# Performance work log

Hardware: AMD Instinct MI355X
Metric: run time of the kernel (lower is better)

The kernel has to match this reference:

```python
import jax, jax.numpy as jnp
import numpy as np

# Config (from ModelConfig in source; num_layers reduced to 4 for the reference)
B, T, D = 4, 8192, 1024
P = 512            # num_patches
S = 4              # patch_stride (OverlapAddDecoder upsample factor)
L = 4              # num transformer layers
NH, NKV, HD = 16, 4, 64
FF = 4096          # ffn_multiplier * D
KC = 256           # MoD capacity = 0.5 * P
V = 257            # vocab_size


def rmsnorm(x, w, eps=1e-6):
    return x * jax.lax.rsqrt(jnp.mean(x * x, -1, keepdims=True) + eps) * w


def rope_cache(n, d):
    theta = 1.0 / (10000.0 ** (jnp.arange(0, d, 2, dtype=jnp.float32) / d))
    fr = jnp.arange(n, dtype=jnp.float32)[:, None] * theta[None, :]
    e = jnp.concatenate([fr, fr], -1)
    return jnp.cos(e), jnp.sin(e)  # (n, d) each


def rot_half(x):
    h = x.shape[-1] // 2
    return jnp.concatenate([-x[..., h:], x[..., :h]], -1)


def setup_inputs() -> dict:
    key = jax.random.key(0)
    ks = iter(jax.random.split(key, 40))
    n = lambda s: jax.random.normal(next(ks), s, dtype=jnp.float32) * 0.02
    return {
        'tokens': jax.random.randint(next(ks), (B, T), 0, V),
        'emb': n((V, D)),
        'bp_w1': n((D // 2, D, 3)), 'bp_b1': jnp.zeros((D // 2,), jnp.float32),
        'bp_w2': n((1, D // 2, 3)), 'bp_b2': jnp.zeros((1,), jnp.float32),
        'enc_norm_w': jnp.ones((D,), jnp.float32),
        'router_w': n((L, D)),
        'ln1_w': jnp.ones((L, D), jnp.float32), 'ln2_w': jnp.ones((L, D), jnp.float32),
        'q_w': n((L, D, D)), 'k_w': n((L, D, NKV * HD)), 'v_w': n((L, D, NKV * HD)), 'o_w': n((L, D, D)),
        'gate_w': n((L, D, FF)), 'up_w': n((L, D, FF)), 'down_w': n((L, FF, D)),
        'dec_proj_w': n((D, S * D)), 'dec_proj_b': jnp.zeros((S * D,), jnp.float32),
        'dec_mlp_w1': n((D, D // 4)), 'dec_mlp_b1': jnp.zeros((D // 4,), jnp.float32),
        'dec_mlp_w2': n((D // 4, S)), 'dec_mlp_b2': jnp.zeros((S,), jnp.float32),
        'dec_norm_w': jnp.ones((D,), jnp.float32),
        'head_w': n((D, V)),
    }


def reference(tokens, emb, bp_w1, bp_b1, bp_w2, bp_b2, enc_norm_w, router_w,
              ln1_w, ln2_w, q_w, k_w, v_w, o_w, gate_w, up_w, down_w,
              dec_proj_w, dec_proj_b, dec_mlp_w1, dec_mlp_b1, dec_mlp_w2, dec_mlp_b2,
              dec_norm_w, head_w):
    x = emb[tokens]  # (B, T, D) byte embeddings

    # --- LearnedBoundaryPredictor: 2-layer 1D CNN -> per-segment soft boundaries ---
    dn = ('NCH', 'OIH', 'NCH')
    xT = x.transpose(0, 2, 1)  # (B, D, T)
    h1 = jax.lax.conv_general_dilated(xT, bp_w1, (1,), ((1, 1),), dimension_numbers=dn) + bp_b1[None, :, None]
    h1 = jax.nn.gelu(h1)
    lg = jax.lax.conv_general_dilated(h1, bp_w2, (1,), ((1, 1),), dimension_numbers=dn) + bp_b2[None, :, None]
    lg = lg[:, 0, :]  # (B, T)

    seg = T // P  # uniform segments (T divisible by P so all segments equal)
    lgw = jax.nn.softmax(lg.reshape(B, P, seg), -1)
    pos = jnp.arange(T, dtype=jnp.float32).reshape(P, seg)
    bp = jnp.sum(lgw * pos[None], -1)                                   # (B, P) soft boundary positions
    ent = -jnp.sum(lgw * jnp.log(jnp.clip(lgw, 1e-8)), -1) / np.log(seg)  # (B, P) entropy signal

    # --- gather patch embeddings at boundary positions, RMSNorm ---
    idx = jnp.clip(bp.astype(jnp.int32), 0, T - 1)
    patches = jnp.take_along_axis(x, idx[..., None], 1)  # (B, P, D)
    xp = rmsnorm(patches, enc_norm_w)

    cos, sin = rope_cache(P, HD)
    b_idx = jnp.arange(B)[:, None]
    causal = jnp.tril(jnp.ones((KC, KC), bool))
    G = NH // NKV

    # --- MoD-routed transformer stack: top-k tokens go through the layer ---
    for l in range(L):
        rl = jnp.einsum('bpd,d->bp', xp, router_w[l]) + ent  # router logits (entropy-boosted)
        _, sel = jax.lax.top_k(rl, KC)
        sel = jnp.sort(sel, -1)  # ascending positions -> causal order preserved
        xs = xp[b_idx, sel]      # (B, KC, D) selected tokens
        g = jax.nn.sigmoid(rl[b_idx, sel])[..., None]  # router gate
        cs = cos[sel][:, None]   # (B, 1, KC, HD)
        sn = sin[sel][:, None]

        # GQA with RoPE, causal
        h = rmsnorm(xs, ln1_w[l])
        q = (h @ q_w[l]).reshape(B, KC, NH, HD).transpose(0, 2, 1, 3)
        k = (h @ k_w[l]).reshape(B, KC, NKV, HD).transpose(0, 2, 1, 3)
        v = (h @ v_w[l]).reshape(B, KC, NKV, HD).transpose(0, 2, 1, 3)
        q = q * cs + rot_half(q) * sn
        k = k * cs + rot_half(k) * sn
        k = jnp.repeat(k, G, axis=1)
        v = jnp.repeat(v, G, axis=1)
        sc = jnp.einsum('bhqd,bhkd->bhqk', q, k) / np.sqrt(HD)
        sc = jnp.where(causal, sc, -1e30)
        a = jax.nn.softmax(sc, -1)
        ao = (jnp.einsum('bhqk,bhkd->bhqd', a, v).transpose(0, 2, 1, 3).reshape(B, KC, D)) @ o_w[l]

        x2 = xs + ao
        h2 = rmsnorm(x2, ln2_w[l])
        ff = (jax.nn.silu(h2 @ gate_w[l]) * (h2 @ up_w[l])) @ down_w[l]
        delta = ao + ff  # layer(x_sel) - x_sel
        xp = xp.at[b_idx, sel].add(g * delta)  # scatter back; unselected pass through

    # --- OverlapAddDecoder ---
    proj = (xp @ dec_proj_w + dec_proj_b).reshape(B, P, S, D)
    win = jax.nn.sigmoid(jax.nn.gelu(xp @ dec_mlp_w1 + dec_mlp_b1) @ dec_mlp_w2 + dec_mlp_b2)  # (B, P, S)
    out = rmsnorm((proj * win[..., None]).reshape(B, P * S, D), dec_norm_w)
    return out @ head_w  # (B, P*S, V) byte logits
```

## Files before the change

kernel.cpp:

```cpp
#include <hip/hip_runtime.h>
#include <hip/hip_bf16.h>
#include <math.h>

constexpr int Bn  = 4;
constexpr int Tn  = 8192;
constexpr int Dn  = 1024;
constexpr int Pn  = 512;
constexpr int SEGn= 16;
constexpr int Sn  = 4;
constexpr int Ln  = 4;
constexpr int NHn = 16;
constexpr int NKVn= 4;
constexpr int HDn = 64;
constexpr int FFn = 4096;
constexpr int KCn = 256;
constexpr int Vn  = 257;
constexpr int DHn = 512;

constexpr long OFF_EW  = 0;
constexpr long OFF_CA  = 394752;
constexpr long OFF_CB  = 427520;
constexpr long OFF_CC  = 460288;
constexpr long OFF_ENT = 493056;
constexpr long OFF_IDX = 495104;
constexpr long OFF_XP  = 497152;
constexpr long OFF_RL  = 2594304;
constexpr long OFF_SEL = 2596352;
constexpr long OFF_G   = 2597376;
constexpr long SCR     = 2598400;
constexpr long SC_XS   = 0;
constexpr long SC_H    = 1048576;
constexpr long SC_QKV  = 2097152;
constexpr long SC_AOUT = 3670016;
constexpr long SC_AO   = 4718592;
constexpr long SC_H2   = 5767168;
constexpr long SC_GU   = 6815744;
constexpr long SC_PROJ = 0;
constexpr long SC_Y    = 8921088;
constexpr long SC_EA   = 0;
constexpr long SC_WB   = 524288;
constexpr long OFF_WT    = 19908096;
constexpr long OFF_PARTS = 24102400;
constexpr long OFF_GHL   = 28820992;

typedef __attribute__((ext_vector_type(8))) short short8;
typedef __attribute__((ext_vector_type(4))) float floatx4;

__device__ __forceinline__ float geluf(float x) {
    float u = 0.7978845608028654f * (x + 0.044715f * x * x * x);
    float e = __expf(2.f * u);
    float t = 1.f - 2.f / (e + 1.f);
    return 0.5f * x * (1.f + t);
}
__device__ __forceinline__ float sigmf(float x) { return 1.f / (1.f + expf(-x)); }

__device__ __forceinline__ void cvt_hilo(float x, unsigned short& h, unsigned short& l) {
    unsigned u = __float_as_uint(x);
    h = (unsigned short)(u >> 16);
    float r = x - __uint_as_float(u & 0xffff0000u);
    l = (unsigned short)(__float_as_uint(r) >> 16);
}

typedef const __attribute__((address_space(1))) unsigned int* gas_p;
typedef __attribute__((address_space(3))) unsigned int* las_p;
__device__ __forceinline__ void gload16(const unsigned short* g, unsigned short* l) {
    __builtin_amdgcn_global_load_lds((gas_p)g, (las_p)l, 16, 0, 0);
}

__device__ __forceinline__ float blk_sum256(float v, float* red) {
    for (int o = 32; o > 0; o >>= 1) v += __shfl_down(v, o);
    int lane = threadIdx.x & 63, w = threadIdx.x >> 6;
    if (lane == 0) red[w] = v;
    __syncthreads();
    float r = red[0] + red[1] + red[2] + red[3];
    __syncthreads();
    return r;
}

__global__ void k_emb_pad(const float* __restrict__ emb, unsigned short* __restrict__ EA) {
    int i = blockIdx.x * blockDim.x + threadIdx.x;
    if (i >= 384 * 1024) return;
    int r = i >> 10, d = i & 1023;
    float v = (r < Vn) ? emb[r * 1024 + d] : 0.f;
    unsigned short hh, ll;
    cvt_hilo(v, hh, ll);
    EA[(long)r * 2048 + d] = hh;
    EA[(long)r * 2048 + 1024 + d] = ll;
}

__global__ void k_wconv_w1(const float* __restrict__ w1, unsigned short* __restrict__ WB) {
    int i = blockIdx.x * blockDim.x + threadIdx.x;
    if (i >= 1536 * 1024) return;
    int n = i >> 10, k = i & 1023;
    float v = w1[(n / 3) * 3072 + k * 3 + (n % 3)];
    unsigned short hh, ll;
    cvt_hilo(v, hh, ll);
    WB[(long)n * 2048 + k] = hh;
    WB[(long)n * 2048 + 1024 + k] = ll;
}

__global__ void k_ewred(const float* __restrict__ parts, float* __restrict__ EW) {
    int i = blockIdx.x * blockDim.x + threadIdx.x;
    if (i >= 3 * Vn * DHn) return;
    int dk = i / (Vn * DHn);
    int rem = i - dk * (Vn * DHn);
    int v = rem >> 9, o = rem & 511;
    long src = (long)v * 1536 + o * 3 + dk;
    float s = 0.f;
    constexpr long MN = 384L * 1536;
    #pragma unroll
    for (int c = 0; c < 8; c++) s += parts[c * MN + src];
    EW[i] = s;
}

__global__ void k_conv1(const int* __restrict__ tok, const float* __restrict__ EW,
                        const float* __restrict__ b1, const float* __restrict__ w2,
                        float* __restrict__ cA, float* __restrict__ cB, float* __restrict__ cC) {
    int wave = threadIdx.x >> 6, lane = threadIdx.x & 63;
    int gidx = blockIdx.x * 4 + wave;
    int b = gidx / Tn, t = gidx - b * Tn;
    int tk  = tok[b * Tn + t];
    int tkm = (t > 0)      ? tok[b * Tn + t - 1] : -1;
    int tkp = (t < Tn - 1) ? tok[b * Tn + t + 1] : -1;
    const float* E0 = EW;
    const float* E1 = EW + (long)Vn * DHn;
    const float* E2 = EW + 2L * Vn * DHn;
    float a0 = 0.f, a1 = 0.f, a2 = 0.f;
    #pragma unroll
    for (int u = 0; u < DHn / 64; u++) {
        int o = lane + u * 64;
        float s = b1[o] + E1[tk * DHn + o];
        if (tkm >= 0) s += E0[tkm * DHn + o];
        if (tkp >= 0) s += E2[tkp * DHn + o];
        float hg = geluf(s);
        a0 += hg * w2[o * 3 + 0];
        a1 += hg * w2[o * 3 + 1];
        a2 += hg * w2[o * 3 + 2];
    }
    for (int o = 32; o > 0; o >>= 1) {
        a0 += __shfl_down(a0, o); a1 += __shfl_down(a1, o); a2 += __shfl_down(a2, o);
    }
    if (lane == 0) { cA[gidx] = a0; cB[gidx] = a1; cC[gidx] = a2; }
}

__global__ void k_patchstats(const float* __restrict__ cA, const float* __restrict__ cB,
                             const float* __restrict__ cC, const float* __restrict__ b2,
                             float* __restrict__ ent_out, int* __restrict__ idx_out) {
    int pid = blockIdx.x * blockDim.x + threadIdx.x;
    if (pid >= Bn * Pn) return;
    int b = pid / Pn, p = pid - b * Pn;
    float lgv[SEGn];
    float m = -3.4e38f;
    for (int s = 0; s < SEGn; s++) {
        int t = p * SEGn + s;
        float v = b2[0] + cB[b * Tn + t];
        if (t > 0)      v += cA[b * Tn + t - 1];
        if (t < Tn - 1) v += cC[b * Tn + t + 1];
        lgv[s] = v; m = fmaxf(m, v);
    }
    float Z = 0.f;
    for (int s = 0; s < SEGn; s++) { lgv[s] = expf(lgv[s] - m); Z += lgv[s]; }
    float inv = 1.f / Z;
    float bp = 0.f, en = 0.f;
    for (int s = 0; s < SEGn; s++) {
        float w = lgv[s] * inv;
        bp += w * (float)(p * SEGn + s);
        en -= w * logf(fmaxf(w, 1e-8f));
    }
    en *= (1.f / 2.772588722239781f);
    ent_out[pid] = en;
    int ix = (int)bp;
    ix = ix < 0 ? 0 : (ix > Tn - 1 ? Tn - 1 : ix);
    idx_out[pid] = ix;
}

__global__ void k_xp(const int* __restrict__ tok, const int* __restrict__ idx,
                     const float* __restrict__ emb, const float* __restrict__ nw,
                     float* __restrict__ xp) {
    int pid = blockIdx.x;
    int b = pid / Pn;
    int tk = tok[b * Tn + idx[pid]];
    const float* row = emb + (long)tk * Dn;
    __shared__ float red[4];
    float v[4]; float ss = 0.f;
    #pragma unroll
    for (int j = 0; j < 4; j++) { v[j] = row[threadIdx.x + j * 256]; ss += v[j] * v[j]; }
    ss = blk_sum256(ss, red);
    float sc = 1.f / sqrtf(ss * (1.f / Dn) + 1e-6f);
    #pragma unroll
    for (int j = 0; j < 4; j++) {
        int d = threadIdx.x + j * 256;
        xp[(long)pid * Dn + d] = v[j] * sc * nw[d];
    }
}

__global__ void k_router(const float* __restrict__ xp, const float* __restrict__ rw,
                         const float* __restrict__ ent, float* __restrict__ rl) {
    int pid = blockIdx.x;
    const float* xr = xp + (long)pid * Dn;
    __shared__ float red[4];
    float s = 0.f;
    #pragma unroll
    for (int j = 0; j < 4; j++) { int d = threadIdx.x + j * 256; s += xr[d] * rw[d]; }
    s = blk_sum256(s, red);
    if (threadIdx.x == 0) rl[pid] = s + ent[pid];
}

__global__ void k_topk(const float* __restrict__ rl, int* __restrict__ sel, float* __restrict__ g) {
    int b = blockIdx.x, p = threadIdx.x;
    __shared__ float vals[Pn];
    __shared__ int flag[Pn];
    float v = rl[b * Pn + p];
    vals[p] = v;
    __syncthreads();
    int rank = 0;
    for (int q = 0; q < Pn; q++) {
        float vq = vals[q];
        rank += (vq > v || (vq == v && q < p)) ? 1 : 0;
    }
    int selected = rank < KCn ? 1 : 0;
    flag[p] = selected;
    __syncthreads();
    if (selected) {
        int pos = 0;
        for (int q = 0; q < p; q++) pos += flag[q];
        sel[b * KCn + pos] = p;
        g[b * KCn + pos] = sigmf(v);
    }
}

__global__ void k_gather_ln1(const float* __restrict__ xp, const int* __restrict__ sel,
                             const float* __restrict__ w, float* __restrict__ xs,
                             unsigned short* __restrict__ hHL) {
    int r = blockIdx.x;
    int b = r / KCn;
    int p = sel[r];
    const float* src = xp + ((long)b * Pn + p) * Dn;
    __shared__ float red[4];
    float v[4]; float ss = 0.f;
    #pragma unroll
    for (int j = 0; j < 4; j++) { v[j] = src[threadIdx.x + j * 256]; ss += v[j] * v[j]; }
    ss = blk_sum256(ss, red);
    float sc = 1.f / sqrtf(ss * (1.f / Dn) + 1e-6f);
    #pragma unroll
    for (int j = 0; j < 4; j++) {
        int d = threadIdx.x + j * 256;
        xs[(long)r * Dn + d] = v[j];
        unsigned short hh, ll;
        cvt_hilo(v[j] * sc * w[d], hh, ll);
        hHL[(long)r * 2048 + d] = hh;
        hHL[(long)r * 2048 + 1024 + d] = ll;
    }
}

__device__ __forceinline__ void wconv_body(const float* __restrict__ Wm,
                                           unsigned short* __restrict__ Whl,
                                           int K, int N, int roff, int n0, int k0) {
    __shared__ float t[32][33];
    int tx = threadIdx.x & 31, ty = threadIdx.x >> 5;
    #pragma unroll
    for (int r = 0; r < 4; r++) {
        int k = k0 + ty + 8 * r, n = n0 + tx;
        t[ty + 8 * r][tx] = (n < N) ? Wm[(long)k * N + n] : 0.f;
    }
    __syncthreads();
    long K2 = 2L * K;
    #pragma unroll
    for (int r = 0; r < 4; r++) {
        int n = n0 + ty + 8 * r, k = k0 + tx;
        float v = t[tx][ty + 8 * r];
        unsigned short hh, ll;
        cvt_hilo(v, hh, ll);
        Whl[(long)(roff + n) * K2 + k] = hh;
        Whl[(long)(roff + n) * K2 + K + k] = ll;
    }
}

__global__ void k_wconv(const float* __restrict__ Wm, unsigned short* __restrict__ Whl,
                        int K, int N, int roff) {
    wconv_body(Wm, Whl, K, N, roff, blockIdx.x * 32, blockIdx.y * 32);
}

__global__ void k_wconv2(const float* __restrict__ Wa, const float* __restrict__ Wb,
                         unsigned short* __restrict__ Whl, int K, int Nh) {
    int nb = Nh >> 5;
    int bx = blockIdx.x;
    const float* src = (bx < nb) ? Wa : Wb;
    int xb = (bx < nb) ? bx : bx - nb;
    int roff = (bx < nb) ? 0 : Nh;
    wconv_body(src, Whl, K, Nh, roff, xb * 32, blockIdx.y * 32);
}

__global__ void k_wconv_qkv(const float* __restrict__ qw, const float* __restrict__ kw,
                            const float* __restrict__ vw, unsigned short* __restrict__ Whl) {
    int bx = blockIdx.x;
    const float* src; int xb, roff, Nsrc;
    if (bx < 32)      { src = qw; xb = bx;      roff = 0;    Nsrc = 1024; }
    else if (bx < 40) { src = kw; xb = bx - 32; roff = 1024; Nsrc = 256; }
    else              { src = vw; xb = bx - 40; roff = 1280; Nsrc = 256; }
    wconv_body(src, Whl, 1024, Nsrc, roff, xb * 32, blockIdx.y * 32);
}

__global__ void k_xcvt(const float* __restrict__ src, unsigned short* __restrict__ dhl, int n) {
    int i = blockIdx.x * blockDim.x + threadIdx.x;
    if (i >= n) return;
    int r = i >> 10, d = i & 1023;
    unsigned short hh, ll;
    cvt_hilo(src[i], hh, ll);
    dhl[(long)r * 2048 + d] = hh;
    dhl[(long)r * 2048 + 1024 + d] = ll;
}

__global__ __launch_bounds__(256, 2) void k_mfma3(
        const unsigned short* __restrict__ Ag, const unsigned short* __restrict__ Bg,
        float* __restrict__ Cmat, const float* __restrict__ bias,
        int M, int N, int K, int splitK, float* __restrict__ parts) {
    __shared__ alignas(16) unsigned short As[2][128 * 64], Bs[2][128 * 64];
    int tid = threadIdx.x;
    int m0 = blockIdx.y * 128, n0 = blockIdx.x * 128;
    int kc = blockIdx.z;
    int Kc = K / splitK, kbase = kc * Kc, KT = Kc >> 5;
    int lane = tid & 63, wid = tid >> 6;
    int wm = (wid & 1) * 64, wn = (wid >> 1) * 64;
    int quad = lane >> 4, l16 = lane & 15;

    int srow8 = lane >> 3;
    int spos  = lane & 7;
    int cch   = spos ^ srow8;
    long K2 = 2L * K;
    long coff = (cch < 4) ? (long)(cch * 8) : (long)K + (long)((cch - 4) * 8);
    const unsigned short* Aseg = Ag + (long)(m0 + srow8) * K2 + coff;
    const unsigned short* Bseg = Bg + (long)(n0 + srow8) * K2 + coff;

    floatx4 acc[4][4];
    #pragma unroll
    for (int i = 0; i < 4; i++)
        #pragma unroll
        for (int j = 0; j < 4; j++) acc[i][j] = (floatx4){0.f, 0.f, 0.f, 0.f};

    auto stagef = [&](unsigned short* Ad, unsigned short* Bd, long kb) {
        #pragma unroll
        for (int t = 0; t < 4; t++) {
            int sa = wid * 4 + t;
            gload16(Aseg + (long)sa * 8 * K2 + kb, Ad + sa * 512);
            gload16(Bseg + (long)sa * 8 * K2 + kb, Bd + sa * 512);
        }
    };

    int ph = quad ^ (l16 & 7);
    stagef(As[0], Bs[0], kbase);
    __syncthreads();
    int cur = 0;
    for (int ks = 0; ks < KT; ks++) {
        if (ks + 1 < KT)
            stagef(As[cur ^ 1], Bs[cur ^ 1], kbase + (long)(ks + 1) * 32);

        const unsigned short* Ac = As[cur];
        const unsigned short* Bc = Bs[cur];
        short8 ah[4], al2[4], bh[4], bl2[4];
        #pragma unroll
        for (int i = 0; i < 4; i++) {
            int r = wm + i * 16 + l16;
            ah[i]  = *(const short8*)&Ac[r * 64 + ph * 8];
            al2[i] = *(const short8*)&Ac[r * 64 + (ph ^ 4) * 8];
        }
        #pragma unroll
        for (int j = 0; j < 4; j++) {
            int c = wn + j * 16 + l16;
            bh[j]  = *(const short8*)&Bc[c * 64 + ph * 8];
            bl2[j] = *(const short8*)&Bc[c * 64 + (ph ^ 4) * 8];
        }
        #pragma unroll
        for (int i = 0; i < 4; i++)
            #pragma unroll
            for (int j = 0; j < 4; j++) {
                acc[i][j] = __builtin_amdgcn_mfma_f32_16x16x32_bf16(ah[i],  bh[j],  acc[i][j], 0, 0, 0);
                acc[i][j] = __builtin_amdgcn_mfma_f32_16x16x32_bf16(ah[i],  bl2[j], acc[i][j], 0, 0, 0);
                acc[i][j] = __builtin_amdgcn_mfma_f32_16x16x32_bf16(al2[i], bh[j],  acc[i][j], 0, 0, 0);
            }
        __syncthreads();
        cur ^= 1;
    }

    long MN = (long)M * N;
    #pragma unroll
    for (int j = 0; j < 4; j++) {
        int n = n0 + wn + j * 16 + l16;
        if (n >= N) continue;
        float bvx = bias ? bias[n] : 0.f;
        #pragma unroll
        for (int i = 0; i < 4; i++) {
            int mb = m0 + wm + i * 16 + quad * 4;
            #pragma unroll
            for (int r = 0; r < 4; r++) {
                if (splitK > 1) parts[kc * MN + (long)(mb + r) * N + n] = acc[i][j][r];
                else            Cmat[(long)(mb + r) * N + n] = acc[i][j][r] + bvx;
            }
        }
    }
}

__global__ void k_reduce(const float* __restrict__ parts, float* __restrict__ out,
                         const float* __restrict__ bias, long MN, int sk, int N) {
    long i = (long)blockIdx.x * blockDim.x + threadIdx.x;
    if (i >= MN) return;
    float s = 0.f;
    for (int c = 0; c < sk; c++) s += parts[c * MN + i];
    if (bias) s += bias[(int)(i % N)];
    out[i] = s;
}

__global__ void k_qkv_finish(const float* __restrict__ parts, const int* __restrict__ sel,
                             float* __restrict__ qkv) {
    int r = blockIdx.x;
    int pos = sel[r];
    constexpr long MN = 1024L * 1536;
    #pragma unroll
    for (int it = 0; it < 3; it++) {
        int pp = threadIdx.x + it * 256;
        int head = pp >> 5, d = pp & 31;
        long c1 = (long)r * 1536 + head * 64 + d;
        float s1 = 0.f, s2 = 0.f;
        #pragma unroll
        for (int c = 0; c < 4; c++) {
            s1 += parts[c * MN + c1];
            s2 += parts[c * MN + c1 + 32];
        }
        if (head < 20) {
            float theta = powf(10000.f, -(float)(2 * d) / 64.f);
            float ang = (float)pos * theta;
            float cc = cosf(ang), ssn = sinf(ang);
            qkv[c1]      = s1 * cc - s2 * ssn;
            qkv[c1 + 32] = s2 * cc + s1 * ssn;
        } else {
            qkv[c1] = s1; qkv[c1 + 32] = s2;
        }
    }
}

constexpr int APS = 72;
__global__ __launch_bounds__(256) void k_attn(const float* __restrict__ qkv,
                       unsigned short* __restrict__ aoHL) {
    int bx = blockIdx.x, h = blockIdx.y, b = blockIdx.z;
    int hk = h >> 2;
    int qb0 = bx * 64;
    int tid = threadIdx.x, lane = tid & 63, wid = tid >> 6;
    int quad = lane >> 4, l16 = lane & 15;
    __shared__ alignas(16) unsigned short LdsA[9216], LdsB[9216];
    unsigned short* Kh = LdsA;          unsigned short* Kl = LdsB;
    unsigned short* Ph = LdsA;          unsigned short* Pl = LdsB;
    unsigned short* Vth = LdsA + 4608;  unsigned short* Vtl = LdsB + 4608;

    int qrow = qb0 + wid * 16 + l16;
    short8 qh[2], ql[2];
    #pragma unroll
    for (int ks = 0; ks < 2; ks++) {
        const float* qp = qkv + ((long)(b * KCn + qrow)) * 1536 + h * HDn + ks * 32 + quad * 8;
        float tmp[8];
        *(float4*)tmp = *(const float4*)qp;
        *(float4*)(tmp + 4) = *(const float4*)(qp + 4);
        #pragma unroll
        for (int j = 0; j < 8; j++) {
            unsigned short hh, ll;
            cvt_hilo(tmp[j], hh, ll);
            qh[ks][j] = (short)hh; ql[ks][j] = (short)ll;
        }
    }

    floatx4 sacc[16];
    #pragma unroll
    for (int t = 0; t < 16; t++) sacc[t] = (floatx4){0.f, 0.f, 0.f, 0.f};

    int qmax = qb0 + 63;
    int nkc = qmax / 128 + 1;
    for (int kc = 0; kc < nkc; kc++) {
        __syncthreads();
        {
            int r = tid >> 1, dh = (tid & 1) * 32;
            const float* kp = qkv + ((long)(b * KCn + kc * 128 + r)) * 1536 + 1024 + hk * HDn + dh;
            #pragma unroll
            for (int f = 0; f < 8; f++) {
                float tmp[4];
                *(float4*)tmp = *(const float4*)(kp + f * 4);
                unsigned short h0, h1, h2, h3, l0, l1, l2, l3;
                cvt_hilo(tmp[0], h0, l0); cvt_hilo(tmp[1], h1, l1);
                cvt_hilo(tmp[2], h2, l2); cvt_hilo(tmp[3], h3, l3);
                *(ushort4*)&Kh[r * APS + dh + f * 4] = make_ushort4(h0, h1, h2, h3);
                *(ushort4*)&Kl[r * APS + dh + f * 4] = make_ushort4(l0, l1, l2, l3);
            }
        }
        __syncthreads();
        #pragma unroll
        for (int tj = 0; tj < 8; tj++) {
            int kr = tj * 16 + l16;
            int gt = kc * 8 + tj;
            #pragma unroll
            for (int ks = 0; ks < 2; ks++) {
                short8 bh0 = *(const short8*)&Kh[kr * APS + ks * 32 + quad * 8];
                short8 bl0 = *(const short8*)&Kl[kr * APS + ks * 32 + quad * 8];
                sacc[gt] = __builtin_amdgcn_mfma_f32_16x16x32_bf16(qh[ks], bh0, sacc[gt], 0, 0, 0);
                sacc[gt] = __builtin_amdgcn_mfma_f32_16x16x32_bf16(qh[ks], bl0, sacc[gt], 0, 0, 0);
                sacc[gt] = __builtin_amdgcn_mfma_f32_16x16x32_bf16(ql[ks], bh0, sacc[gt], 0, 0, 0);
            }
        }
    }

    float rowinv[4];
    #pragma unroll
    for (int r = 0; r < 4; r++) {
        int qg = qb0 + wid * 16 + quad * 4 + r;
        float mm = -3.4e38f;
        #pragma unroll
        for (int t = 0; t < 16; t++) {
            int key = t * 16 + l16;
            float s = (key <= qg) ? sacc[t][r] * 0.125f : -1e30f;
            sacc[t][r] = s;
            mm = fmaxf(mm, s);
        }
        #pragma unroll
        for (int o = 1; o < 16; o <<= 1) mm = fmaxf(mm, __shfl_xor(mm, o));
        float zz = 0.f;
        #pragma unroll
        for (int t = 0; t < 16; t++) {
            float e = expf(sacc[t][r] - mm);
            sacc[t][r] = e; zz += e;
        }
        #pragma unroll
        for (int o = 1; o < 16; o <<= 1) zz += __shfl_xor(zz, o);
        rowinv[r] = 1.f / zz;
    }

    floatx4 oacc[4];
    #pragma unroll
    for (int dt = 0; dt < 4; dt++) oacc[dt] = (floatx4){0.f, 0.f, 0.f, 0.f};
    int npv = qmax / 64 + 1;
    for (int c4 = 0; c4 < npv; c4++) {
        __syncthreads();
        {
            #pragma unroll
            for (int it = 0; it < 4; it++) {
                int task = tid + 256 * it;
                int kloc = task & 63, d4 = (task >> 6) * 4;
                float tmp[4];
                *(float4*)tmp = *(const float4*)(qkv + ((long)(b * KCn + c4 * 64 + kloc)) * 1536 + 1280 + hk * HDn + d4);
                #pragma unroll
                for (int i = 0; i < 4; i++) {
                    unsigned short hh, ll;
                    cvt_hilo(tmp[i], hh, ll);
                    Vth[(d4 + i) * APS + kloc] = hh;
                    Vtl[(d4 + i) * APS + kloc] = ll;
                }
            }
        }
        #pragma unroll
        for (int tt = 0; tt < 4; tt++) {
            int t = c4 * 4 + tt;
            #pragma unroll
            for (int r = 0; r < 4; r++) {
                int row = wid * 16 + quad * 4 + r;
                float pv2 = sacc[t][r] * rowinv[r];
                unsigned short hh, ll;
                cvt_hilo(pv2, hh, ll);
                Ph[row * APS + tt * 16 + l16] = hh;
                Pl[row * APS + tt * 16 + l16] = ll;
            }
        }
        __syncthreads();
        short8 pah[2], pal[2];
        #pragma unroll
        for (int ks = 0; ks < 2; ks++) {
            pah[ks] = *(const short8*)&Ph[(wid * 16 + l16) * APS + ks * 32 + quad * 8];
            pal[ks] = *(const short8*)&Pl[(wid * 16 + l16) * APS + ks * 32 + quad * 8];
        }
        #pragma unroll
        for (int dt = 0; dt < 4; dt++) {
            #pragma unroll
            for (int ks = 0; ks < 2; ks++) {
                short8 vbh = *(const short8*)&Vth[(dt * 16 + l16) * APS + ks * 32 + quad * 8];
                short8 vbl = *(const short8*)&Vtl[(dt * 16 + l16) * APS + ks * 32 + quad * 8];
                oacc[dt] = __builtin_amdgcn_mfma_f32_16x16x32_bf16(pah[ks], vbh, oacc[dt], 0, 0, 0);
                oacc[dt] = __builtin_amdgcn_mfma_f32_16x16x32_bf16(pah[ks], vbl, oacc[dt], 0, 0, 0);
                oacc[dt] = __builtin_amdgcn_mfma_f32_16x16x32_bf16(pal[ks], vbh, oacc[dt], 0, 0, 0);
            }
        }
    }

    #pragma unroll
    for (int dt = 0; dt < 4; dt++) {
        #pragma unroll
        for (int r = 0; r < 4; r++) {
            int row = qb0 + wid * 16 + quad * 4 + r;
            long base = ((long)(b * KCn + row)) * 2048 + h * HDn + dt * 16 + l16;
            unsigned short hh, ll;
            cvt_hilo(oacc[dt][r], hh, ll);
            aoHL[base] = hh; aoHL[base + 1024] = ll;
        }
    }
}

__global__ void k_add_ln2_red(const float* __restrict__ parts, const float* __restrict__ xs,
                              const float* __restrict__ w, float* __restrict__ ao,
                              unsigned short* __restrict__ h2HL) {
    int r = blockIdx.x;
    constexpr long MN = 1024L * 1024;
    __shared__ float red[4];
    float v[4]; float ss = 0.f;
    #pragma unroll
    for (int j = 0; j < 4; j++) {
        int d = threadIdx.x + j * 256;
        long i = (long)r * Dn + d;
        float a = 0.f;
        #pragma unroll
        for (int c = 0; c < 8; c++) a += parts[c * MN + i];
        ao[i] = a;
        float x = xs[i] + a;
        v[j] = x; ss += x * x;
    }
    ss = blk_sum256(ss, red);
    float sc = 1.f / sqrtf(ss * (1.f / Dn) + 1e-6f);
    #pragma unroll
    for (int j = 0; j < 4; j++) {
        int d = threadIdx.x + j * 256;
        unsigned short hh, ll;
        cvt_hilo(v[j] * sc * w[d], hh, ll);
        h2HL[(long)r * 2048 + d] = hh;
        h2HL[(long)r * 2048 + 1024 + d] = ll;
    }
}

__global__ void k_silu_mul(const float* __restrict__ C, unsigned short* __restrict__ ghl, int n) {
    int i = blockIdx.x * blockDim.x + threadIdx.x;
    if (i < n) {
        int r = i >> 12, c = i & 4095;
        float x = C[(long)r * 8192 + c];
        float u = C[(long)r * 8192 + 4096 + c];
        unsigned short hh, ll;
        cvt_hilo(x * sigmf(x) * u, hh, ll);
        ghl[(long)r * 8192 + c] = hh;
        ghl[(long)r * 8192 + 4096 + c] = ll;
    }
}

__global__ void k_scatter_red(float* __restrict__ xp, const float* __restrict__ ao,
                              const float* __restrict__ parts, const float* __restrict__ g,
                              const int* __restrict__ sel) {
    int r = blockIdx.x;
    int b = r / KCn;
    int p = sel[r];
    float gg = g[r];
    constexpr long MN = 1024L * 1024;
    float* dst = xp + ((long)b * Pn + p) * Dn;
    #pragma unroll
    for (int j = 0; j < 4; j++) {
        int d = threadIdx.x + j * 256;
        long i = (long)r * Dn + d;
        float f = 0.f;
        #pragma unroll
        for (int c = 0; c < 4; c++) f += parts[c * MN + i];
        dst[d] += gg * (ao[i] + f);
    }
}

__global__ void k_dec_norm_win(const float* __restrict__ projC, const float* __restrict__ mparts,
                               const float* __restrict__ b1, const float* __restrict__ w2,
                               const float* __restrict__ b2, const float* __restrict__ w,
                               unsigned short* __restrict__ yHL) {
    int r = blockIdx.x;
    int bp = r >> 2, s = r & 3;
    constexpr long MN = 2048L * 256;
    __shared__ float red[4];
    long hi = (long)bp * 256 + threadIdx.x;
    float hv = b1[threadIdx.x];
    #pragma unroll
    for (int c = 0; c < 4; c++) hv += mparts[c * MN + hi];
    float acc = geluf(hv) * w2[threadIdx.x * 4 + s];
    acc = blk_sum256(acc, red);
    float wv = sigmf(acc + b2[s]);
    const float* pr = projC + (long)bp * 4096 + s * 1024;
    float v[4]; float ss = 0.f;
    #pragma unroll
    for (int j = 0; j < 4; j++) {
        int d = threadIdx.x + j * 256;
        float x = pr[d] * wv;
        v[j] = x; ss += x * x;
    }
    ss = blk_sum256(ss, red);
    float sc = 1.f / sqrtf(ss * (1.f / Dn) + 1e-6f);
    #pragma unroll
    for (int j = 0; j < 4; j++) {
        int d = threadIdx.x + j * 256;
        unsigned short hh, ll;
        cvt_hilo(v[j] * sc * w[d], hh, ll);
        yHL[(long)r * 2048 + d] = hh;
        yHL[(long)r * 2048 + 1024 + d] = ll;
    }
}

extern "C" void kernel_launch(void* const* d_in, const int* in_sizes, int n_in,
                              void* d_out, int out_size, void* d_ws, size_t ws_size,
                              hipStream_t stream) {
    const int*   tokens     = (const int*)  d_in[0];
    const float* emb        = (const float*)d_in[1];
    const float* bp_w1      = (const float*)d_in[2];
    const float* bp_b1      = (const float*)d_in[3];
    const float* bp_w2      = (const float*)d_in[4];
    const float* bp_b2      = (const float*)d_in[5];
    const float* enc_norm_w = (const float*)d_in[6];
    const float* router_w   = (const float*)d_in[7];
    const float* ln1_w      = (const float*)d_in[8];
    const float* ln2_w      = (const float*)d_in[9];
    const float* q_w        = (const float*)d_in[10];
    const float* k_w        = (const float*)d_in[11];
    const float* v_w        = (const float*)d_in[12];
    const float* o_w        = (const float*)d_in[13];
    const float* gate_w     = (const float*)d_in[14];
    const float* up_w       = (const float*)d_in[15];
    const float* down_w     = (const float*)d_in[16];
    const float* dec_proj_w = (const float*)d_in[17];
    const float* dec_proj_b = (const float*)d_in[18];
    const float* dec_mlp_w1 = (const float*)d_in[19];
    const float* dec_mlp_b1 = (const float*)d_in[20];
    const float* dec_mlp_w2 = (const float*)d_in[21];
    const float* dec_mlp_b2 = (const float*)d_in[22];
    const float* dec_norm_w = (const float*)d_in[23];
    const float* head_w     = (const float*)d_in[24];
    float* out = (float*)d_out;

    float* W = (float*)d_ws;
    float* EW   = W + OFF_EW;
    float* cA   = W + OFF_CA;
    float* cB   = W + OFF_CB;
    float* cC   = W + OFF_CC;
    float* ent  = W + OFF_ENT;
    int*   idxb = (int*)(W + OFF_IDX);
    float* xp   = W + OFF_XP;
    float* rl   = W + OFF_RL;
    int*   sel  = (int*)(W + OFF_SEL);
    float* g    = W + OFF_G;
    float* scr  = W + SCR;
    float* xs   = scr + SC_XS;
    unsigned short* hHL   = (unsigned short*)(scr + SC_H);
    float* qkv  = scr + SC_QKV;
    unsigned short* aoutHL = (unsigned short*)(scr + SC_AOUT);
    float* ao   = scr + SC_AO;
    unsigned short* h2HL  = (unsigned short*)(scr + SC_H2);
    float* gupC = scr + SC_GU;
    float* projC= scr + SC_PROJ;
    unsigned short* yHL   = (unsigned short*)(scr + SC_Y);
    unsigned short* EA    = (unsigned short*)(scr + SC_EA);
    unsigned short* WB    = (unsigned short*)(scr + SC_WB);
    unsigned short* WHL   = (unsigned short*)(W + OFF_WT);
    float* parts = W + OFF_PARTS;
    unsigned short* ghHL  = (unsigned short*)(W + OFF_GHL);
    unsigned short* xpHL  = (unsigned short*)(W + OFF_GHL);

    k_emb_pad<<<1536, 256, 0, stream>>>(emb, EA);
    k_wconv_w1<<<6144, 256, 0, stream>>>(bp_w1, WB);
    k_mfma3<<<dim3(12, 3, 8), 256, 0, stream>>>(EA, WB, nullptr, nullptr, 384, 1536, 1024, 8, parts);
    k_ewred<<<1542, 256, 0, stream>>>(parts, EW);
    k_conv1<<<Bn * Tn / 4, 256, 0, stream>>>(tokens, EW, bp_b1, bp_w2, cA, cB, cC);
    k_patchstats<<<(Bn * Pn + 255) / 256, 256, 0, stream>>>(cA, cB, cC, bp_b2, ent, idxb);
    k_xp<<<Bn * Pn, 256, 0, stream>>>(tokens, idxb, emb, enc_norm_w, xp);

    for (int l = 0; l < Ln; l++) {
        k_router<<<Bn * Pn, 256, 0, stream>>>(xp, router_w + (long)l * Dn, ent, rl);
        k_topk<<<Bn, Pn, 0, stream>>>(rl, sel, g);
        k_gather_ln1<<<Bn * KCn, 256, 0, stream>>>(xp, sel, ln1_w + (long)l * Dn, xs, hHL);

        k_wconv_qkv<<<dim3(48, 32), 256, 0, stream>>>(q_w + (long)l * Dn * Dn,
                                                      k_w + (long)l * Dn * 256,
                                                      v_w + (long)l * Dn * 256, WHL);
        k_mfma3<<<dim3(12, 8, 4), 256, 0, stream>>>(hHL, WHL, nullptr, nullptr, 1024, 1536, 1024, 4, parts);
        k_qkv_finish<<<Bn * KCn, 256, 0, stream>>>(parts, sel, qkv);

        k_attn<<<dim3(4, NHn, Bn), 256, 0, stream>>>(qkv, aoutHL);

        k_wconv<<<dim3(32, 32), 256, 0, stream>>>(o_w + (long)l * Dn * Dn, WHL, 1024, 1024, 0);
        k_mfma3<<<dim3(8, 8, 8), 256, 0, stream>>>(aoutHL, WHL, nullptr, nullptr, 1024, 1024, 1024, 8, parts);
        k_add_ln2_red<<<Bn * KCn, 256, 0, stream>>>(parts, xs, ln2_w + (long)l * Dn, ao, h2HL);

        k_wconv2<<<dim3(256, 32), 256, 0, stream>>>(gate_w + (long)l * Dn * FFn,
                                                    up_w + (long)l * Dn * FFn, WHL, 1024, 4096);
        k_mfma3<<<dim3(64, 8, 1), 256, 0, stream>>>(h2HL, WHL, gupC, nullptr, 1024, 8192, 1024, 1, parts);

        k_silu_mul<<<(Bn * KCn * FFn + 255) / 256, 256, 0, stream>>>(gupC, ghHL, Bn * KCn * FFn);

        k_wconv<<<dim3(32, 128), 256, 0, stream>>>(down_w + (long)l * FFn * Dn, WHL, 4096, 1024, 0);
        k_mfma3<<<dim3(8, 8, 4), 256, 0, stream>>>(ghHL, WHL, nullptr, nullptr, 1024, 1024, 4096, 4, parts);
        k_scatter_red<<<Bn * KCn, 256, 0, stream>>>(xp, ao, parts, g, sel);
    }

    k_xcvt<<<8192, 256, 0, stream>>>(xp, xpHL, 2097152);
    k_wconv<<<dim3(128, 32), 256, 0, stream>>>(dec_proj_w, WHL, 1024, 4096, 0);
    k_mfma3<<<dim3(32, 16, 1), 256, 0, stream>>>(xpHL, WHL, projC, dec_proj_b, 2048, 4096, 1024, 1, parts);
    k_wconv<<<dim3(8, 32), 256, 0, stream>>>(dec_mlp_w1, WHL, 1024, 256, 0);
    k_mfma3<<<dim3(2, 16, 4), 256, 0, stream>>>(xpHL, WHL, nullptr, nullptr, 2048, 256, 1024, 4, parts);
    k_dec_norm_win<<<Bn * Pn * Sn, 256, 0, stream>>>(projC, parts, dec_mlp_b1, dec_mlp_w2, dec_mlp_b2, dec_norm_w, yHL);
    k_wconv<<<dim3(9, 32), 256, 0, stream>>>(head_w, WHL, 1024, 257, 0);
    k_mfma3<<<dim3(3, 64, 2), 256, 0, stream>>>(yHL, WHL, nullptr, nullptr, 8192, 257, 1024, 2, parts);
    k_reduce<<<8224, 256, 0, stream>>>(parts, out, nullptr, 2105344, 2, 257);
}
```

Baseline: 1.437 ms.

## Store QKV pre-split as bf16 hi/lo, vectorize SiLU, raise down-proj split-K

k_qkv_finish now writes Q, K and V directly as bf16 hi/lo pairs in a split layout, so the attention kernel loads them with short8 copies instead of converting fp32 per element. The SiLU-mul kernel is vectorized to process four elements per thread. The down-projection GEMM goes from split-K 4 to 8, writing its partials into the gupC buffer, and the scatter reduction is updated to sum 8 partials. This trades extra partial-sum traffic for more parallelism in the down-projection, and relies on gupC being free to reuse at that point.

```diff
diff --git a/kernel.cpp b/kernel.cpp
--- a/kernel.cpp
+++ b/kernel.cpp
@@ -411,7 +411,7 @@
 }
 
 __global__ void k_qkv_finish(const float* __restrict__ parts, const int* __restrict__ sel,
-                             float* __restrict__ qkv) {
+                             unsigned short* __restrict__ qkvHL) {
     int r = blockIdx.x;
     int pos = sel[r];
     constexpr long MN = 1024L * 1536;
@@ -426,20 +426,33 @@
             s1 += parts[c * MN + c1];
             s2 += parts[c * MN + c1 + 32];
         }
+        float o1, o2;
         if (head < 20) {
             float theta = powf(10000.f, -(float)(2 * d) / 64.f);
             float ang = (float)pos * theta;
             float cc = cosf(ang), ssn = sinf(ang);
-            qkv[c1]      = s1 * cc - s2 * ssn;
-            qkv[c1 + 32] = s2 * cc + s1 * ssn;
+            o1 = s1 * cc - s2 * ssn;
+            o2 = s2 * cc + s1 * ssn;
         } else {
-            qkv[c1] = s1; qkv[c1 + 32] = s2;
-        }
+            o1 = s1; o2 = s2;
+        }
+        long hb, lb; int dloc;
+        if (head < 16)      { hb = 0;    lb = 1024; dloc = head * 64 + d; }
+        else if (head < 20) { hb = 2048; lb = 2304; dloc = (head - 16) * 64 + d; }
+        else                { hb = 2560; lb = 2816; dloc = (head - 20) * 64 + d; }
+        long base = (long)r * 3072;
+        unsigned short h1, l1, h2, l2;
+        cvt_hilo(o1, h1, l1);
+        cvt_hilo(o2, h2, l2);
+        qkvHL[base + hb + dloc]      = h1;
+        qkvHL[base + lb + dloc]      = l1;
+        qkvHL[base + hb + dloc + 32] = h2;
+        qkvHL[base + lb + dloc + 32] = l2;
     }
 }
 
 constexpr int APS = 72;
-__global__ __launch_bounds__(256) void k_attn(const float* __restrict__ qkv,
+__global__ __launch_bounds__(256) void k_attn(const unsigned short* __restrict__ qkvHL,
                        unsigned short* __restrict__ aoHL) {
     int bx = blockIdx.x, h = blockIdx.y, b = blockIdx.z;
     int hk = h >> 2;
@@ -455,16 +468,9 @@
     short8 qh[2], ql[2];
     #pragma unroll
     for (int ks = 0; ks < 2; ks++) {
-        const float* qp = qkv + ((long)(b * KCn + qrow)) * 1536 + h * HDn + ks * 32 + quad * 8;
-        float tmp[8];
-        *(float4*)tmp = *(const float4*)qp;
-        *(float4*)(tmp + 4) = *(const float4*)(qp + 4);
-        #pragma unroll
-        for (int j = 0; j < 8; j++) {
-            unsigned short hh, ll;
-            cvt_hilo(tmp[j], hh, ll);
-            qh[ks][j] = (short)hh; ql[ks][j] = (short)ll;
-        }
+        const unsigned short* qp = qkvHL + ((long)(b * KCn + qrow)) * 3072 + h * HDn + ks * 32 + quad * 8;
+        qh[ks] = *(const short8*)qp;
+        ql[ks] = *(const short8*)(qp + 1024);
     }
 
     floatx4 sacc[16];
@@ -477,16 +483,11 @@
         __syncthreads();
         {
             int r = tid >> 1, dh = (tid & 1) * 32;
-            const float* kp = qkv + ((long)(b * KCn + kc * 128 + r)) * 1536 + 1024 + hk * HDn + dh;
+            const unsigned short* kp = qkvHL + ((long)(b * KCn + kc * 128 + r)) * 3072 + 2048 + hk * HDn + dh;
             #pragma unroll
-            for (int f = 0; f < 8; f++) {
-                float tmp[4];
-                *(float4*)tmp = *(const float4*)(kp + f * 4);
-                unsigned short h0, h1, h2, h3, l0, l1, l2, l3;
-                cvt_hilo(tmp[0], h0, l0); cvt_hilo(tmp[1], h1, l1);
-                cvt_hilo(tmp[2], h2, l2); cvt_hilo(tmp[3], h3, l3);
-                *(ushort4*)&Kh[r * APS + dh + f * 4] = make_ushort4(h0, h1, h2, h3);
-                *(ushort4*)&Kl[r * APS + dh + f * 4] = make_ushort4(l0, l1, l2, l3);
+            for (int f = 0; f < 4; f++) {
+                *(short8*)&Kh[r * APS + dh + f * 8] = *(const short8*)(kp + f * 8);
+                *(short8*)&Kl[r * APS + dh + f * 8] = *(const short8*)(kp + 256 + f * 8);
             }
         }
         __syncthreads();
@@ -541,15 +542,13 @@
             for (int it = 0; it < 4; it++) {
                 int task = tid + 256 * it;
                 int kloc = task & 63, d4 = (task >> 6) * 4;
-                float tmp[4];
-                *(float4*)tmp = *(const float4*)(qkv + ((long)(b * KCn + c4 * 64 + kloc)) * 1536 + 1280 + hk * HDn + d4);
-                #pragma unroll
-                for (int i = 0; i < 4; i++) {
-                    unsigned short hh, ll;
-                    cvt_hilo(tmp[i], hh, ll);
-                    Vth[(d4 + i) * APS + kloc] = hh;
-                    Vtl[(d4 + i) * APS + kloc] = ll;
-                }
+                const unsigned short* vp = qkvHL + ((long)(b * KCn + c4 * 64 + kloc)) * 3072 + 2560 + hk * HDn + d4;
+                ushort4 th = *(const ushort4*)vp;
+                ushort4 tl = *(const ushort4*)(vp + 256);
+                Vth[(d4 + 0) * APS + kloc] = th.x; Vtl[(d4 + 0) * APS + kloc] = tl.x;
+                Vth[(d4 + 1) * APS + kloc] = th.y; Vtl[(d4 + 1) * APS + kloc] = tl.y;
+                Vth[(d4 + 2) * APS + kloc] = th.z; Vtl[(d4 + 2) * APS + kloc] = tl.z;
+                Vth[(d4 + 3) * APS + kloc] = th.w; Vtl[(d4 + 3) * APS + kloc] = tl.w;
             }
         }
         #pragma unroll
@@ -628,17 +627,21 @@
     }
 }
 
-__global__ void k_silu_mul(const float* __restrict__ C, unsigned short* __restrict__ ghl, int n) {
+__global__ void k_silu_mul(const float* __restrict__ C, unsigned short* __restrict__ ghl, int n4) {
     int i = blockIdx.x * blockDim.x + threadIdx.x;
-    if (i < n) {
-        int r = i >> 12, c = i & 4095;
-        float x = C[(long)r * 8192 + c];
-        float u = C[(long)r * 8192 + 4096 + c];
-        unsigned short hh, ll;
-        cvt_hilo(x * sigmf(x) * u, hh, ll);
-        ghl[(long)r * 8192 + c] = hh;
-        ghl[(long)r * 8192 + 4096 + c] = ll;
-    }
+    if (i >= n4) return;
+    int i4 = i << 2;
+    int r = i4 >> 12, c = i4 & 4095;
+    float4 x = *(const float4*)&C[(long)r * 8192 + c];
+    float4 u = *(const float4*)&C[(long)r * 8192 + 4096 + c];
+    ushort4 oh, ol;
+    unsigned short hh, ll;
+    cvt_hilo(x.x * sigmf(x.x) * u.x, hh, ll); oh.x = hh; ol.x = ll;
+    cvt_hilo(x.y * sigmf(x.y) * u.y, hh, ll); oh.y = hh; ol.y = ll;
+    cvt_hilo(x.z * sigmf(x.z) * u.z, hh, ll); oh.z = hh; ol.z = ll;
+    cvt_hilo(x.w * sigmf(x.w) * u.w, hh, ll); oh.w = hh; ol.w = ll;
+    *(ushort4*)&ghl[(long)r * 8192 + c] = oh;
+    *(ushort4*)&ghl[(long)r * 8192 + 4096 + c] = ol;
 }
 
 __global__ void k_scatter_red(float* __restrict__ xp, const float* __restrict__ ao,
@@ -656,7 +659,7 @@
         long i = (long)r * Dn + d;
         float f = 0.f;
         #pragma unroll
-        for (int c = 0; c < 4; c++) f += parts[c * MN + i];
+        for (int c = 0; c < 8; c++) f += parts[c * MN + i];
         dst[d] += gg * (ao[i] + f);
     }
 }
@@ -740,7 +743,7 @@
     float* scr  = W + SCR;
     float* xs   = scr + SC_XS;
     unsigned short* hHL   = (unsigned short*)(scr + SC_H);
-    float* qkv  = scr + SC_QKV;
+    unsigned short* qkvHL = (unsigned short*)(scr + SC_QKV);
     unsigned short* aoutHL = (unsigned short*)(scr + SC_AOUT);
     float* ao   = scr + SC_AO;
     unsigned short* h2HL  = (unsigned short*)(scr + SC_H2);
@@ -771,9 +774,9 @@
                                                       k_w + (long)l * Dn * 256,
                                                       v_w + (long)l * Dn * 256, WHL);
         k_mfma3<<<dim3(12, 8, 4), 256, 0, stream>>>(hHL, WHL, nullptr, nullptr, 1024, 1536, 1024, 4, parts);
-        k_qkv_finish<<<Bn * KCn, 256, 0, stream>>>(parts, sel, qkv);
-
-        k_attn<<<dim3(4, NHn, Bn), 256, 0, stream>>>(qkv, aoutHL);
+        k_qkv_finish<<<Bn * KCn, 256, 0, stream>>>(parts, sel, qkvHL);
+
+        k_attn<<<dim3(4, NHn, Bn), 256, 0, stream>>>(qkvHL, aoutHL);
 
         k_wconv<<<dim3(32, 32), 256, 0, stream>>>(o_w + (long)l * Dn * Dn, WHL, 1024, 1024, 0);
         k_mfma3<<<dim3(8, 8, 8), 256, 0, stream>>>(aoutHL, WHL, nullptr, nullptr, 1024, 1024, 1024, 8, parts);
@@ -783,11 +786,11 @@
                                                     up_w + (long)l * Dn * FFn, WHL, 1024, 4096);
         k_mfma3<<<dim3(64, 8, 1), 256, 0, stream>>>(h2HL, WHL, gupC, nullptr, 1024, 8192, 1024, 1, parts);
 
-        k_silu_mul<<<(Bn * KCn * FFn + 255) / 256, 256, 0, stream>>>(gupC, ghHL, Bn * KCn * FFn);
+        k_silu_mul<<<(Bn * KCn * FFn / 4 + 255) / 256, 256, 0, stream>>>(gupC, ghHL, Bn * KCn * FFn / 4);
 
         k_wconv<<<dim3(32, 128), 256, 0, stream>>>(down_w + (long)l * FFn * Dn, WHL, 4096, 1024, 0);
-        k_mfma3<<<dim3(8, 8, 4), 256, 0, stream>>>(ghHL, WHL, nullptr, nullptr, 1024, 1024, 4096, 4, parts);
-        k_scatter_red<<<Bn * KCn, 256, 0, stream>>>(xp, ao, parts, g, sel);
+        k_mfma3<<<dim3(8, 8, 8), 256, 0, stream>>>(ghHL, WHL, nullptr, nullptr, 1024, 1024, 4096, 8, gupC);
+        k_scatter_red<<<Bn * KCn, 256, 0, stream>>>(xp, ao, gupC, g, sel);
     }
 
     k_xcvt<<<8192, 256, 0, stream>>>(xp, xpHL, 2097152);
```

Result: no change. 1.415 ms (-1.5%).
